# Kernel tuning notes

Measured on AMD Instinct MI355X. Metric: run time of the kernel, lower is better.

Reference implementation:

```python
import jax, jax.numpy as jnp
import numpy as np

ALPHA = 1000.0


def setup_inputs() -> dict:
    key = jax.random.key(0)
    inputs = jax.random.normal(key, (8, 1024, 16), dtype=jnp.float32)
    return {"inputs": inputs}


def reference(inputs) -> jnp.ndarray:
    # SoftRank (training path):
    # out[b, j, c] = (1/N) * sum_i sigmoid(alpha * (x[b, j, c] - x[b, i, c]))
    x = inputs  # [B, N, C]
    n = x.shape[1]
    # diff[b, j, i, c] = x[b, j, c] - x[b, i, c]
    diff = x[:, :, None, :] - x[:, None, :, :]  # [B, N, N, C]
    out = jnp.sum(jax.nn.sigmoid(ALPHA * diff), axis=2) / jnp.asarray(n, x.dtype)
    return out  # [B, N, C]
```

## Files before the change

kernel.cpp:

```cpp
#include <hip/hip_runtime.h>


#define K_LOG2E 1442.6950408889634f

constexpr int Bdim = 8;
constexpr int Ndim = 1024;
constexpr int Cdim = 16;
constexpr int NB   = 1024;
constexpr float RANGE = 6.0f;

__global__ __launch_bounds__(1024)
void softrank_bucket(const float* __restrict__ x, float* __restrict__ out) {
    __shared__ int   cnt[NB];
    __shared__ int   cum[NB];
    __shared__ int   off[NB];
    __shared__ float sv[Ndim];

    const int t = threadIdx.x;
    const int b = blockIdx.x >> 4;
    const int c = blockIdx.x & 15;

    const float v = K_LOG2E * x[b * (Ndim * Cdim) + t * Cdim + c];

    const float inv_w = (float)NB / (2.0f * RANGE * K_LOG2E);
    int k = (int)floorf((v + RANGE * K_LOG2E) * inv_w);
    k = min(max(k, 0), NB - 1);

    cnt[t] = 0;
    __syncthreads();
    atomicAdd(&cnt[k], 1);
    __syncthreads();

    const int myc = cnt[t];
    cum[t] = myc;
    __syncthreads();
    for (int d = 1; d < NB; d <<= 1) {
        int add = (t >= d) ? cum[t - d] : 0;
        __syncthreads();
        cum[t] += add;
        __syncthreads();
    }

    off[t] = cum[t] - myc;
    __syncthreads();
    int pos = atomicAdd(&off[k], 1);
    sv[pos] = v;
    __syncthreads();

    const int lo = (k >= 2) ? cum[k - 2] : 0;
    const int hi = (k + 1 <= NB - 1) ? cum[k + 1] : Ndim;

    float acc = 0.0f;
    for (int p = lo; p < hi; ++p) {
        float u = v - sv[p];
        float e = __builtin_amdgcn_exp2f(-u);
        acc += __builtin_amdgcn_rcpf(1.0f + e);
    }

    out[b * (Ndim * Cdim) + t * Cdim + c] = ((float)lo + acc) * (1.0f / (float)Ndim);
}

extern "C" void kernel_launch(void* const* d_in, const int* in_sizes, int n_in,
                              void* d_out, int out_size, void* d_ws, size_t ws_size,
                              hipStream_t stream) {
    (void)in_sizes; (void)n_in; (void)d_ws; (void)ws_size; (void)out_size;
    const float* x = (const float*)d_in[0];
    float* out = (float*)d_out;
    softrank_bucket<<<Bdim * Cdim, 1024, 0, stream>>>(x, out);
}
```

Before: 56.93 us.

## Process four elements per thread and replace block scan with wave-shuffle scan

Shrinks each block from 1024 to 256 threads, with every thread handling four elements. The 10-step shared-memory prefix scan, which needed about twenty block barriers, is replaced by a vectorised int4 per-thread scan, a wave-level shuffle scan and a small cross-wave fixup. The aim is to remove most of the barrier and shared-memory traffic overhead. In exchange each block has fewer waves to hide latency, and each thread runs its four neighbour-sum loops one after another.

```diff
diff --git a/kernel.cpp b/kernel.cpp
--- a/kernel.cpp
+++ b/kernel.cpp
@@ -8,56 +8,81 @@
 constexpr int Cdim = 16;
 constexpr int NB   = 1024;
 constexpr float RANGE = 6.0f;
+constexpr int THREADS = 256;
 
-__global__ __launch_bounds__(1024)
-void softrank_bucket(const float* __restrict__ x, float* __restrict__ out) {
+__global__ __launch_bounds__(THREADS)
+void softrank_bucket3(const float* __restrict__ x, float* __restrict__ out) {
     __shared__ int   cnt[NB];
     __shared__ int   cum[NB];
     __shared__ int   off[NB];
     __shared__ float sv[Ndim];
+    __shared__ int   wpart[4];
 
-    const int t = threadIdx.x;
+    const int t    = threadIdx.x;
+    const int w    = t >> 6;
+    const int lane = t & 63;
     const int b = blockIdx.x >> 4;
     const int c = blockIdx.x & 15;
 
-    const float v = K_LOG2E * x[b * (Ndim * Cdim) + t * Cdim + c];
+    const float* xb = x + b * (Ndim * Cdim) + c;
 
     const float inv_w = (float)NB / (2.0f * RANGE * K_LOG2E);
-    int k = (int)floorf((v + RANGE * K_LOG2E) * inv_w);
-    k = min(max(k, 0), NB - 1);
+    float v[4]; int k[4];
+    #pragma unroll
+    for (int u = 0; u < 4; ++u) {
+        const int e = t + THREADS * u;
+        v[u] = K_LOG2E * xb[e * Cdim];
+        int kk = (int)floorf((v[u] + RANGE * K_LOG2E) * inv_w);
+        k[u] = min(max(kk, 0), NB - 1);
+    }
 
-    cnt[t] = 0;
+    ((int4*)cnt)[t] = make_int4(0, 0, 0, 0);
     __syncthreads();
-    atomicAdd(&cnt[k], 1);
+    #pragma unroll
+    for (int u = 0; u < 4; ++u) atomicAdd(&cnt[k[u]], 1);
     __syncthreads();
 
-    const int myc = cnt[t];
-    cum[t] = myc;
+    int4 c4 = ((const int4*)cnt)[t];
+    int s0 = c4.x, s1 = s0 + c4.y, s2 = s1 + c4.z, s3 = s2 + c4.w;
+    int ws = s3;
+    #pragma unroll
+    for (int d = 1; d < 64; d <<= 1) {
+        int n = __shfl_up(ws, d, 64);
+        if (lane >= d) ws += n;
+    }
+    const int wexcl = ws - s3;
+    if (lane == 63) wpart[w] = ws;
     __syncthreads();
-    for (int d = 1; d < NB; d <<= 1) {
-        int add = (t >= d) ? cum[t - d] : 0;
-        __syncthreads();
-        cum[t] += add;
-        __syncthreads();
-    }
-
-    off[t] = cum[t] - myc;
-    __syncthreads();
-    int pos = atomicAdd(&off[k], 1);
-    sv[pos] = v;
+    int base = wexcl;
+    if (w > 0) base += wpart[0];
+    if (w > 1) base += wpart[1];
+    if (w > 2) base += wpart[2];
+    ((int4*)cum)[t] = make_int4(base + s0, base + s1, base + s2, base + s3);
+    ((int4*)off)[t] = make_int4(base, base + s0, base + s1, base + s2);
     __syncthreads();
 
-    const int lo = (k >= 2) ? cum[k - 2] : 0;
-    const int hi = (k + 1 <= NB - 1) ? cum[k + 1] : Ndim;
+    int pos[4];
+    #pragma unroll
+    for (int u = 0; u < 4; ++u) {
+        pos[u] = atomicAdd(&off[k[u]], 1);
+        sv[pos[u]] = v[u];
+    }
+    __syncthreads();
 
-    float acc = 0.0f;
-    for (int p = lo; p < hi; ++p) {
-        float u = v - sv[p];
-        float e = __builtin_amdgcn_exp2f(-u);
-        acc += __builtin_amdgcn_rcpf(1.0f + e);
+    #pragma unroll
+    for (int u = 0; u < 4; ++u) {
+        const int lo = (k[u] >= 2) ? cum[k[u] - 2] : 0;
+        const int hi = cum[min(k[u] + 1, NB - 1)];
+        float acc = 0.0f;
+        for (int p = lo; p < hi; ++p) {
+            float d2 = v[u] - sv[p];
+            float e2 = __builtin_amdgcn_exp2f(-d2);
+            acc += __builtin_amdgcn_rcpf(1.0f + e2);
+        }
+        const int e = t + THREADS * u;
+        out[b * (Ndim * Cdim) + e * Cdim + c] =
+            ((float)lo + acc) * (1.0f / (float)Ndim);
     }
-
-    out[b * (Ndim * Cdim) + t * Cdim + c] = ((float)lo + acc) * (1.0f / (float)Ndim);
 }
 
 extern "C" void kernel_launch(void* const* d_in, const int* in_sizes, int n_in,
@@ -66,5 +91,5 @@
     (void)in_sizes; (void)n_in; (void)d_ws; (void)ws_size; (void)out_size;
     const float* x = (const float*)d_in[0];
     float* out = (float*)d_out;
-    softrank_bucket<<<Bdim * Cdim, 1024, 0, stream>>>(x, out);
+    softrank_bucket3<<<Bdim * Cdim, THREADS, 0, stream>>>(x, out);
 }
```

Measured after the change: 59.99 us. 1.05x slower.
